# Kernel optimization log

Hardware: AMD Instinct MI355X
Metric: run time of the kernel (lower is better)

## Reference

```python
import jax, jax.numpy as jnp
import numpy as np

B, S, D, H = 4, 1024, 1024, 16
DH = D // H  # head dim 64
DFF = 4 * D


def _lin(x, w, b):
    # torch nn.Linear: x @ W^T + b, W: [out, in]
    return x @ w.T + b


def _heads(x):
    # [B,S,D] -> [B,H,S,DH]
    b, s, _ = x.shape
    return x.reshape(b, s, H, DH).transpose(0, 2, 1, 3)


def setup_inputs() -> dict:
    key = jax.random.key(0)
    ks = iter(jax.random.split(key, 32))

    def w(shape):
        return jax.random.normal(next(ks), shape, jnp.float32) * 0.02

    inp = {
        "global_feat": jax.random.normal(next(ks), (B, S, D), jnp.float32),
        "local_feat": jax.random.normal(next(ks), (B, S, D), jnp.float32),
        "text_feat": jax.random.normal(next(ks), (B, S, D), jnp.float32),
    }
    # embedding blocks (build) and all projections: D x D linears
    for name in ["ge", "le1", "le2", "qg", "kg", "vg", "qp", "kp", "vp", "dense", "ml"]:
        inp[name + "_w"] = w((D, D))
        inp[name + "_b"] = w((D,))
    # MLP: D -> 4D -> D
    inp["fc1_w"] = w((DFF, D)); inp["fc1_b"] = w((DFF,))
    inp["fc2_w"] = w((D, DFF)); inp["fc2_b"] = w((D,))
    return inp


def reference(global_feat, local_feat, text_feat,
              ge_w, ge_b, le1_w, le1_b, le2_w, le2_b,
              qg_w, qg_b, kg_w, kg_b, vg_w, vg_b,
              qp_w, qp_b, kp_w, kp_b, vp_w, vp_b,
              dense_w, dense_b, ml_w, ml_b,
              fc1_w, fc1_b, fc2_w, fc2_b):
    b, s, d = global_feat.shape
    scale = 1.0 / jnp.sqrt(jnp.asarray(DH, global_feat.dtype))

    # embeddings (build blocks; dropout = identity in eval)
    dup_local = _lin(local_feat, le1_w, le1_b)
    local = _lin(local_feat, le2_w, le2_b)
    glob = _lin(global_feat, ge_w, ge_b)

    # global branch: Q from global, K/V from local
    qg = _heads(_lin(glob, qg_w, qg_b))
    kg = _heads(_lin(local, kg_w, kg_b))
    vg = _heads(_lin(local, vg_w, vg_b))
    # local branch: Q from duplicated local, K/V from text
    qp = _heads(_lin(dup_local, qp_w, qp_b))
    kp = _heads(_lin(text_feat, kp_w, kp_b))
    vp = _heads(_lin(text_feat, vp_w, vp_b))

    glb_probs = jax.nn.softmax(jnp.einsum("bhqd,bhkd->bhqk", qg, kg) * scale, axis=-1)
    plb_probs = jax.nn.softmax(jnp.einsum("bhqd,bhkd->bhqk", qp, kp) * scale, axis=-1)

    # bridge: probs @ probs (the non-standard O(S^3) stage)
    plb_enh = jnp.einsum("bhqk,bhks->bhqs", glb_probs, plb_probs)

    glb_ctx = jnp.einsum("bhqk,bhkd->bhqd", glb_probs, vg)
    plb_ctx = jnp.einsum("bhqs,bhsd->bhqd", plb_enh, vp)

    def merge(x):
        return x.transpose(0, 2, 1, 3).reshape(b, s, d)

    last = merge(glb_ctx) + merge(plb_ctx)
    out = _lin(last, dense_w, dense_b)
    # MLP: D -> 4D -> D with GELU
    out = _lin(jax.nn.gelu(_lin(out, fc1_w, fc1_b), approximate=False), fc2_w, fc2_b)
    out = _lin(out, ml_w, ml_b)
    return out
```

## Files before the change

kernel.cpp:

```cpp
#include <hip/hip_runtime.h>
#include <cstdint>
#include <cstddef>

#define B_   4
#define S_   1024
#define D_   1024
#define H_   16
#define DH_  64
#define DFF_ 4096
#define M_   (B_ * S_)

typedef __bf16 bf16x8 __attribute__((ext_vector_type(8)));
typedef float  f32x4  __attribute__((ext_vector_type(4)));

__device__ __forceinline__ unsigned short f2bf(float f) {
  unsigned int u = __float_as_uint(f);
  u = (u + 0x7fffu + ((u >> 16) & 1u)) >> 16;
  return (unsigned short)u;
}

__device__ __forceinline__ float bf2f(unsigned short h) {
  return __uint_as_float(((unsigned int)h) << 16);
}

__device__ __forceinline__ void gload_lds16(const void* g, void* l) {
  __builtin_amdgcn_global_load_lds((const __attribute__((address_space(1))) void*)g,
                                   (__attribute__((address_space(3))) void*)l, 16, 0, 0);
}

#define NCVT 16
struct CvtB { const float* s[NCVT]; unsigned short* d[NCVT]; int n[NCVT]; };

__global__ __launch_bounds__(256)
void cvt_k(CvtB cb) {
  const int z = blockIdx.y;
  const float* __restrict__ s = cb.s[z];
  unsigned short* __restrict__ d = cb.d[z];
  const int n = cb.n[z];
  const int stride = gridDim.x * 256 * 4;
  for (int i = (blockIdx.x * 256 + threadIdx.x) * 4; i < n; i += stride) {
    const float4 v = *(const float4*)(s + i);
    const unsigned int a = (unsigned int)f2bf(v.x) | ((unsigned int)f2bf(v.y) << 16);
    const unsigned int b = (unsigned int)f2bf(v.z) | ((unsigned int)f2bf(v.w) << 16);
    *(uint2*)(d + i) = make_uint2(a, b);
  }
}

#define MAXB 6
struct GemmB {
  const unsigned short* A[MAXB];
  const unsigned short* W[MAXB];
  const float*          bias[MAXB];
  void*                 Y[MAXB];
};

template <int GELU, int OUTF32>
__global__ __launch_bounds__(256)
void mgemm(GemmB gb, int M, int N, int K) {
  __shared__ unsigned short sA[128][32];
  __shared__ unsigned short sB[128][32];

  const int z = blockIdx.z;
  const unsigned short* __restrict__ A = gb.A[z];
  const unsigned short* __restrict__ W = gb.W[z];
  const float* __restrict__ bias = gb.bias[z];

  const int t  = threadIdx.x;
  const int ln = t & 63;
  const int wv = t >> 6;
  const int wr = wv >> 1;
  const int wc = wv & 1;
  const int m0 = blockIdx.y * 128;
  const int n0 = blockIdx.x * 128;

  const int srow  = ln >> 2;
  const int skoff = (ln & 3) << 3;

  f32x4 acc[4][4] = {};

  char* sAb = (char*)&sA[0][0];
  char* sBb = (char*)&sB[0][0];

  for (int k0 = 0; k0 < K; k0 += 32) {
    __syncthreads();
#pragma unroll
    for (int i = 0; i < 2; ++i) {
      const int c = (wv << 1) | i;
      gload_lds16(A + (size_t)(m0 + (c << 4) + srow) * K + k0 + skoff, sAb + (c << 10));
      gload_lds16(W + (size_t)(n0 + (c << 4) + srow) * K + k0 + skoff, sBb + (c << 10));
    }
    __syncthreads();

    const int rsel = ln & 15;
    const int csel = (ln >> 4) << 4;
    bf16x8 av[4], bv[4];
#pragma unroll
    for (int m = 0; m < 4; ++m)
      av[m] = *(const bf16x8*)(sAb + (((wr << 6) + (m << 4) + rsel) << 6) + csel);
#pragma unroll
    for (int n = 0; n < 4; ++n)
      bv[n] = *(const bf16x8*)(sBb + (((wc << 6) + (n << 4) + rsel) << 6) + csel);

#pragma unroll
    for (int m = 0; m < 4; ++m)
#pragma unroll
      for (int n = 0; n < 4; ++n)
        acc[m][n] = __builtin_amdgcn_mfma_f32_16x16x32_bf16(av[m], bv[n], acc[m][n], 0, 0, 0);
  }

  const int rbase = m0 + (wr << 6) + ((ln >> 4) << 2);
  const int cb0   = n0 + (wc << 6) + (ln & 15);
#pragma unroll
  for (int m = 0; m < 4; ++m) {
#pragma unroll
    for (int n = 0; n < 4; ++n) {
      const int col = cb0 + (n << 4);
      const float bi = bias[col];
#pragma unroll
      for (int j = 0; j < 4; ++j) {
        const int row = rbase + (m << 4) + j;
        float x = acc[m][n][j] + bi;
        if (GELU) x = 0.5f * x * (1.0f + erff(x * 0.70710678118654752f));
        if (OUTF32) ((float*)gb.Y[z])[(size_t)row * N + col] = x;
        else        ((unsigned short*)gb.Y[z])[(size_t)row * N + col] = f2bf(x);
      }
    }
  }
}

__global__ __launch_bounds__(256)
void vtrans_k(const unsigned short* __restrict__ V, unsigned short* __restrict__ Vt) {
  const int t   = threadIdx.x;
  const int d   = t & 63;
  const int sub = t >> 6;
  const int bh  = blockIdx.y;
  const int b   = bh >> 4;
  const int col0 = (bh & 15) * DH_;
  const int kv0 = blockIdx.x * 32 + sub * 8;
  unsigned short tmp[8];
#pragma unroll
  for (int i = 0; i < 8; ++i)
    tmp[i] = V[((size_t)b * S_ + kv0 + i) * D_ + col0 + d];
  *(uint4*)(Vt + ((size_t)bh * DH_ + d) * S_ + kv0) = *(const uint4*)tmp;
}

__global__ __launch_bounds__(256)
void attn_mfma_k(const unsigned short* __restrict__ Q,
                 const unsigned short* __restrict__ K,
                 const unsigned short* __restrict__ Vt,
                 const unsigned short* __restrict__ addend,
                 unsigned short* __restrict__ O) {
  __shared__ unsigned short sQ[64 * 64];
  __shared__ unsigned short sK[64 * 64];
  __shared__ unsigned short sV[64 * 64];
  __shared__ unsigned short sP[4][16 * 72];

  const int t  = threadIdx.x;
  const int l  = t & 63;
  const int w  = t >> 6;
  const int bh = blockIdx.y;
  const int b  = bh >> 4;
  const size_t rowQ = (size_t)b * S_ + blockIdx.x * 64;
  const size_t rowK = (size_t)b * S_;
  const int col0 = (bh & 15) * DH_;

  const int lr8 = l >> 3;
  const int lsw = (l & 7) ^ lr8;
  char* sQb = (char*)sQ;
  char* sKb = (char*)sK;
  char* sVb = (char*)sV;

#pragma unroll
  for (int i = 0; i < 2; ++i) {
    const int r = w * 16 + i * 8 + lr8;
    gload_lds16(Q + (rowQ + r) * D_ + col0 + lsw * 8, sQb + w * 2048 + i * 1024);
    gload_lds16(K + (rowK + r) * D_ + col0 + lsw * 8, sKb + w * 2048 + i * 1024);
    gload_lds16(Vt + ((size_t)bh * DH_ + r) * S_ + lsw * 8, sVb + w * 2048 + i * 1024);
  }
  __syncthreads();

  bf16x8 qa[2];
#pragma unroll
  for (int c = 0; c < 2; ++c)
    qa[c] = *(const bf16x8*)(sQb + (w * 16 + (l & 15)) * 128 +
                             ((((c << 2) + (l >> 4)) ^ (l & 7)) << 4));

  f32x4 o[4] = {};
  float mrow[4] = {-1e30f, -1e30f, -1e30f, -1e30f};
  float lrow[4] = {0.f, 0.f, 0.f, 0.f};

  char* sPw = (char*)(sP[w]);

  for (int kt = 0; kt < S_ / 64; ++kt) {
    f32x4 s[4];
#pragma unroll
    for (int n = 0; n < 4; ++n) {
      f32x4 z = {};
#pragma unroll
      for (int c = 0; c < 2; ++c) {
        const bf16x8 kb = *(const bf16x8*)(sKb + (n * 16 + (l & 15)) * 128 +
                              ((((c << 2) + (l >> 4)) ^ (l & 7)) << 4));
        z = __builtin_amdgcn_mfma_f32_16x16x32_bf16(qa[c], kb, z, 0, 0, 0);
      }
      s[n] = z;
    }

#pragma unroll
    for (int j = 0; j < 4; ++j) {
      float rm = fmaxf(fmaxf(s[0][j], s[1][j]), fmaxf(s[2][j], s[3][j]));
      rm = fmaxf(rm, __shfl_xor(rm, 1));
      rm = fmaxf(rm, __shfl_xor(rm, 2));
      rm = fmaxf(rm, __shfl_xor(rm, 4));
      rm = fmaxf(rm, __shfl_xor(rm, 8));
      const float mn = fmaxf(mrow[j], rm * 0.125f);
      const float cr = __expf(mrow[j] - mn);
      mrow[j] = mn;
      float rs = 0.f;
#pragma unroll
      for (int n = 0; n < 4; ++n) {
        const float p = __expf(s[n][j] * 0.125f - mn);
        rs += p;
        ((unsigned short*)sPw)[((l >> 4) * 4 + j) * 72 + n * 16 + (l & 15)] = f2bf(p);
      }
      rs += __shfl_xor(rs, 1);
      rs += __shfl_xor(rs, 2);
      rs += __shfl_xor(rs, 4);
      rs += __shfl_xor(rs, 8);
      lrow[j] = lrow[j] * cr + rs;
#pragma unroll
      for (int n2 = 0; n2 < 4; ++n2) o[n2][j] *= cr;
    }

    bf16x8 pa[2];
#pragma unroll
    for (int kc = 0; kc < 2; ++kc)
      pa[kc] = *(const bf16x8*)(sPw + (l & 15) * 144 + kc * 64 + (l >> 4) * 16);
#pragma unroll
    for (int n2 = 0; n2 < 4; ++n2) {
#pragma unroll
      for (int kc = 0; kc < 2; ++kc) {
        const bf16x8 vb = *(const bf16x8*)(sVb + (n2 * 16 + (l & 15)) * 128 +
                               ((((kc << 2) + (l >> 4)) ^ (l & 7)) << 4));
        o[n2] = __builtin_amdgcn_mfma_f32_16x16x32_bf16(pa[kc], vb, o[n2], 0, 0, 0);
      }
    }

    __syncthreads();
    if (kt + 1 < S_ / 64) {
#pragma unroll
      for (int i = 0; i < 2; ++i) {
        const int r = w * 16 + i * 8 + lr8;
        gload_lds16(K + (rowK + (size_t)(kt + 1) * 64 + r) * D_ + col0 + lsw * 8,
                    sKb + w * 2048 + i * 1024);
        gload_lds16(Vt + ((size_t)bh * DH_ + r) * S_ + (kt + 1) * 64 + lsw * 8,
                    sVb + w * 2048 + i * 1024);
      }
    }
    __syncthreads();
  }

  float inv[4];
#pragma unroll
  for (int j = 0; j < 4; ++j) inv[j] = 1.f / lrow[j];
#pragma unroll
  for (int n2 = 0; n2 < 4; ++n2) {
#pragma unroll
    for (int j = 0; j < 4; ++j) {
      const size_t row = rowQ + w * 16 + (l >> 4) * 4 + j;
      const int col = col0 + n2 * 16 + (l & 15);
      float x = o[n2][j] * inv[j];
      if (addend != nullptr) x += bf2f(addend[row * D_ + col]);
      O[row * D_ + col] = f2bf(x);
    }
  }
}

extern "C" void kernel_launch(void* const* d_in, const int* in_sizes, int n_in,
                              void* d_out, int out_size, void* d_ws, size_t ws_size,
                              hipStream_t stream) {
  const float* gf = (const float*)d_in[0];
  const float* lf = (const float*)d_in[1];
  const float* tf = (const float*)d_in[2];
  const float* ge_w  = (const float*)d_in[3],  *ge_b  = (const float*)d_in[4];
  const float* le1_w = (const float*)d_in[5],  *le1_b = (const float*)d_in[6];
  const float* le2_w = (const float*)d_in[7],  *le2_b = (const float*)d_in[8];
  const float* qg_w  = (const float*)d_in[9],  *qg_b  = (const float*)d_in[10];
  const float* kg_w  = (const float*)d_in[11], *kg_b  = (const float*)d_in[12];
  const float* vg_w  = (const float*)d_in[13], *vg_b  = (const float*)d_in[14];
  const float* qp_w  = (const float*)d_in[15], *qp_b  = (const float*)d_in[16];
  const float* kp_w  = (const float*)d_in[17], *kp_b  = (const float*)d_in[18];
  const float* vp_w  = (const float*)d_in[19], *vp_b  = (const float*)d_in[20];
  const float* dense_w = (const float*)d_in[21], *dense_b = (const float*)d_in[22];
  const float* ml_w  = (const float*)d_in[23], *ml_b  = (const float*)d_in[24];
  const float* fc1_w = (const float*)d_in[25], *fc1_b = (const float*)d_in[26];
  const float* fc2_w = (const float*)d_in[27], *fc2_b = (const float*)d_in[28];

  float* out = (float*)d_out;

  char* p = (char*)d_ws;
  auto take = [&](size_t bytes) { char* r = p; p += (bytes + 255) & ~(size_t)255; return r; };
  const size_t WD  = (size_t)D_ * D_;
  const size_t WF  = (size_t)DFF_ * D_;
  const size_t ACT = (size_t)M_ * D_;
  const size_t HB  = (size_t)M_ * DFF_;

  unsigned short* wge    = (unsigned short*)take(WD * 2);
  unsigned short* wle1   = (unsigned short*)take(WD * 2);
  unsigned short* wle2   = (unsigned short*)take(WD * 2);
  unsigned short* wqg    = (unsigned short*)take(WD * 2);
  unsigned short* wkg    = (unsigned short*)take(WD * 2);
  unsigned short* wvg    = (unsigned short*)take(WD * 2);
  unsigned short* wqp    = (unsigned short*)take(WD * 2);
  unsigned short* wkp    = (unsigned short*)take(WD * 2);
  unsigned short* wvp    = (unsigned short*)take(WD * 2);
  unsigned short* wdense = (unsigned short*)take(WD * 2);
  unsigned short* wml    = (unsigned short*)take(WD * 2);
  unsigned short* wfc1   = (unsigned short*)take(WF * 2);
  unsigned short* wfc2   = (unsigned short*)take(WF * 2);
  unsigned short* gfb    = (unsigned short*)take(ACT * 2);
  unsigned short* lfb    = (unsigned short*)take(ACT * 2);
  unsigned short* tfb    = (unsigned short*)take(ACT * 2);
  unsigned short* glob   = (unsigned short*)take(ACT * 2);
  unsigned short* loc    = (unsigned short*)take(ACT * 2);
  unsigned short* dup    = (unsigned short*)take(ACT * 2);
  unsigned short* qgb    = (unsigned short*)take(ACT * 2);
  unsigned short* kgb    = (unsigned short*)take(ACT * 2);
  unsigned short* vgb    = (unsigned short*)take(ACT * 2);
  unsigned short* qpb    = (unsigned short*)take(ACT * 2);
  unsigned short* kpb    = (unsigned short*)take(ACT * 2);
  unsigned short* vpb    = (unsigned short*)take(ACT * 2);
  unsigned short* ub     = (unsigned short*)take(ACT * 2);
  unsigned short* lastb  = (unsigned short*)take(ACT * 2);
  unsigned short* out1   = (unsigned short*)take(ACT * 2);
  unsigned short* hbuf   = (unsigned short*)take(HB * 2);
  unsigned short* out2   = (unsigned short*)take(ACT * 2);

  unsigned short* vt1 = gfb;
  unsigned short* vtu = lfb;

  CvtB cb;
  const float* srcs[NCVT] = {ge_w, le1_w, le2_w, qg_w, kg_w, vg_w, qp_w, kp_w, vp_w,
                             dense_w, ml_w, fc1_w, fc2_w, gf, lf, tf};
  unsigned short* dsts[NCVT] = {wge, wle1, wle2, wqg, wkg, wvg, wqp, wkp, wvp,
                                wdense, wml, wfc1, wfc2, gfb, lfb, tfb};
  const int lens[NCVT] = {(int)WD,(int)WD,(int)WD,(int)WD,(int)WD,(int)WD,(int)WD,(int)WD,(int)WD,
                          (int)WD,(int)WD,(int)WF,(int)WF,(int)ACT,(int)ACT,(int)ACT};
  for (int i = 0; i < NCVT; ++i) { cb.s[i] = srcs[i]; cb.d[i] = dsts[i]; cb.n[i] = lens[i]; }
  hipLaunchKernelGGL(cvt_k, dim3(512, NCVT), dim3(256), 0, stream, cb);

  const dim3 blk(256);
  auto mkb = [](std::initializer_list<const unsigned short*> As,
                std::initializer_list<const unsigned short*> Ws,
                std::initializer_list<const float*> Bs,
                std::initializer_list<void*> Ys) {
    GemmB g{};
    int i = 0;
    auto a = As.begin(); auto w = Ws.begin(); auto b = Bs.begin(); auto y = Ys.begin();
    for (; a != As.end(); ++a, ++w, ++b, ++y, ++i) { g.A[i] = *a; g.W[i] = *w; g.bias[i] = *b; g.Y[i] = *y; }
    return g;
  };

  GemmB s1 = mkb({gfb, lfb, lfb}, {wge, wle1, wle2}, {ge_b, le1_b, le2_b},
                 {glob, dup, loc});
  hipLaunchKernelGGL((mgemm<0,0>), dim3(D_/128, M_/128, 3), blk, 0, stream, s1, M_, D_, D_);

  GemmB s2 = mkb({glob, loc, loc, dup, tfb, tfb}, {wqg, wkg, wvg, wqp, wkp, wvp},
                 {qg_b, kg_b, vg_b, qp_b, kp_b, vp_b}, {qgb, kgb, vgb, qpb, kpb, vpb});
  hipLaunchKernelGGL((mgemm<0,0>), dim3(D_/128, M_/128, 6), blk, 0, stream, s2, M_, D_, D_);

  hipLaunchKernelGGL(vtrans_k, dim3(32, 64), blk, 0, stream, vpb, vt1);
  hipLaunchKernelGGL(attn_mfma_k, dim3(16, 64), blk, 0, stream, qpb, kpb, vt1, vgb, ub);
  hipLaunchKernelGGL(vtrans_k, dim3(32, 64), blk, 0, stream, ub, vtu);
  hipLaunchKernelGGL(attn_mfma_k, dim3(16, 64), blk, 0, stream, qgb, kgb, vtu,
                     (const unsigned short*)nullptr, lastb);

  GemmB gd = mkb({lastb}, {wdense}, {dense_b}, {out1});
  hipLaunchKernelGGL((mgemm<0,0>), dim3(D_/128, M_/128, 1), blk, 0, stream, gd, M_, D_, D_);
  GemmB g1 = mkb({out1}, {wfc1}, {fc1_b}, {hbuf});
  hipLaunchKernelGGL((mgemm<1,0>), dim3(DFF_/128, M_/128, 1), blk, 0, stream, g1, M_, DFF_, D_);
  GemmB g2 = mkb({hbuf}, {wfc2}, {fc2_b}, {out2});
  hipLaunchKernelGGL((mgemm<0,0>), dim3(D_/128, M_/128, 1), blk, 0, stream, g2, M_, D_, DFF_);
  GemmB gm = mkb({out2}, {wml}, {ml_b}, {out});
  hipLaunchKernelGGL((mgemm<0,1>), dim3(D_/128, M_/128, 1), blk, 0, stream, gm, M_, D_, D_);
}
```

Before: 653.6 us.

## Double-buffer LDS tiles in batched GEMM and remap workgroups across XCDs

Splits the GEMM shared-memory tiles into two buffers so the next K-slice's global-to-LDS loads are issued before the MFMA work on the current slice. The aim is to overlap load latency with compute instead of serialising them. It also remaps the linear workgroup id so consecutive tiles land on the same XCD, which should improve L2 reuse of A and W. In exchange it doubles LDS use per block, which may lower occupancy, and the unrolled-by-two loop assumes the number of K tiles is even.

Measured after the change: 599.4 us. 8.3% less time.

```diff
diff --git a/kernel.cpp b/kernel.cpp
--- a/kernel.cpp
+++ b/kernel.cpp
@@ -57,8 +57,8 @@
 template <int GELU, int OUTF32>
 __global__ __launch_bounds__(256)
 void mgemm(GemmB gb, int M, int N, int K) {
-  __shared__ unsigned short sA[128][32];
-  __shared__ unsigned short sB[128][32];
+  __shared__ unsigned short sA0[128][32], sA1[128][32];
+  __shared__ unsigned short sB0[128][32], sB1[128][32];
 
   const int z = blockIdx.z;
   const unsigned short* __restrict__ A = gb.A[z];
@@ -70,42 +70,61 @@
   const int wv = t >> 6;
   const int wr = wv >> 1;
   const int wc = wv & 1;
-  const int m0 = blockIdx.y * 128;
-  const int n0 = blockIdx.x * 128;
+
+  const int gx   = gridDim.x;
+  const int nwg  = gx * gridDim.y;
+  const int orig = blockIdx.y * gx + blockIdx.x;
+  const int q8   = nwg >> 3, r8 = nwg & 7;
+  const int xcd  = orig & 7, idx = orig >> 3;
+  const int wgid = (xcd < r8 ? xcd * (q8 + 1) : r8 * (q8 + 1) + (xcd - r8) * q8) + idx;
+  const int m0 = (wgid / gx) * 128;
+  const int n0 = (wgid % gx) * 128;
 
   const int srow  = ln >> 2;
   const int skoff = (ln & 3) << 3;
 
   f32x4 acc[4][4] = {};
 
-  char* sAb = (char*)&sA[0][0];
-  char* sBb = (char*)&sB[0][0];
-
-  for (int k0 = 0; k0 < K; k0 += 32) {
-    __syncthreads();
+  char* a0 = (char*)&sA0[0][0];  char* a1 = (char*)&sA1[0][0];
+  char* b0 = (char*)&sB0[0][0];  char* b1 = (char*)&sB1[0][0];
+
+  const int rsel = ln & 15;
+  const int csel = (ln >> 4) << 4;
+
+  auto stage = [&](int kt, char* dstA, char* dstB) {
+    const int k0 = kt << 5;
 #pragma unroll
     for (int i = 0; i < 2; ++i) {
       const int c = (wv << 1) | i;
-      gload_lds16(A + (size_t)(m0 + (c << 4) + srow) * K + k0 + skoff, sAb + (c << 10));
-      gload_lds16(W + (size_t)(n0 + (c << 4) + srow) * K + k0 + skoff, sBb + (c << 10));
-    }
-    __syncthreads();
-
-    const int rsel = ln & 15;
-    const int csel = (ln >> 4) << 4;
+      gload_lds16(A + (size_t)(m0 + (c << 4) + srow) * K + k0 + skoff, dstA + (c << 10));
+      gload_lds16(W + (size_t)(n0 + (c << 4) + srow) * K + k0 + skoff, dstB + (c << 10));
+    }
+  };
+
+  auto compute = [&](const char* srcA, const char* srcB) {
     bf16x8 av[4], bv[4];
 #pragma unroll
     for (int m = 0; m < 4; ++m)
-      av[m] = *(const bf16x8*)(sAb + (((wr << 6) + (m << 4) + rsel) << 6) + csel);
+      av[m] = *(const bf16x8*)(srcA + (((wr << 6) + (m << 4) + rsel) << 6) + csel);
 #pragma unroll
     for (int n = 0; n < 4; ++n)
-      bv[n] = *(const bf16x8*)(sBb + (((wc << 6) + (n << 4) + rsel) << 6) + csel);
-
+      bv[n] = *(const bf16x8*)(srcB + (((wc << 6) + (n << 4) + rsel) << 6) + csel);
 #pragma unroll
     for (int m = 0; m < 4; ++m)
 #pragma unroll
       for (int n = 0; n < 4; ++n)
         acc[m][n] = __builtin_amdgcn_mfma_f32_16x16x32_bf16(av[m], bv[n], acc[m][n], 0, 0, 0);
+  };
+
+  const int NK = K >> 5;
+  stage(0, a0, b0);
+  for (int kt = 0; kt < NK; kt += 2) {
+    __syncthreads();
+    stage(kt + 1, a1, b1);
+    compute(a0, b0);
+    __syncthreads();
+    if (kt + 2 < NK) stage(kt + 2, a0, b0);
+    compute(a1, b1);
   }
 
   const int rbase = m0 + (wr << 6) + ((ln >> 4) << 2);
```
